# Kernel optimization log

Measured on AMD Instinct MI355X. Metric: run time of the kernel, lower is better.

Reference implementation:

```python
import jax, jax.numpy as jnp
import numpy as np

N_NODES = 200   # nlim = 50*4
EMB = 5
N_APPTYPES = 3
FEAT_IN = 50 * 52 + N_NODES  # 2800
B = 16384
E = 800


def setup_inputs() -> dict:
    key = jax.random.key(0)
    ks = jax.random.split(key, 16)
    x = jax.random.normal(ks[0], (B, 50, 52), dtype=jnp.float32)
    apps = jax.random.randint(ks[1], (B, N_NODES), 0, N_APPTYPES)
    edge_src = jax.random.randint(ks[2], (E,), 0, N_NODES)
    edge_dst = jax.random.randint(ks[3], (E,), 0, N_NODES)
    def lin(k, fan_in, fan_out):
        bound = 1.0 / np.sqrt(fan_in)
        kw, kb = jax.random.split(k)
        W = jax.random.uniform(kw, (fan_in, fan_out), minval=-bound, maxval=bound, dtype=jnp.float32)
        b = jax.random.uniform(kb, (fan_out,), minval=-bound, maxval=bound, dtype=jnp.float32)
        return W, b
    emb_table = jax.random.normal(ks[4], (N_APPTYPES, EMB), dtype=jnp.float32)
    gc_w, gc_b = lin(ks[5], EMB, 1)
    W1, b1 = lin(ks[6], FEAT_IN, 128)
    W2, b2 = lin(ks[7], 128, 128)
    W3, b3 = lin(ks[8], 128, 64)
    W4, b4 = lin(ks[9], 64, 2)
    return {"x": x, "apps": apps, "edge_src": edge_src, "edge_dst": edge_dst,
            "emb_table": emb_table, "gc_w": gc_w, "gc_b": gc_b,
            "W1": W1, "b1": b1, "W2": W2, "b2": b2,
            "W3": W3, "b3": b3, "W4": W4, "b4": b4}


def _graph_conv(h, edge_src, edge_dst, gc_w, gc_b):
    # DGL GraphConv, norm='both': D_in^{-1/2} A D_out^{-1/2} (X W) + b
    ones = jnp.ones((edge_src.shape[0],), dtype=h.dtype)
    deg_out = jnp.clip(jax.ops.segment_sum(ones, edge_src, num_segments=N_NODES), 1.0)
    deg_in = jnp.clip(jax.ops.segment_sum(ones, edge_dst, num_segments=N_NODES), 1.0)
    norm_src = deg_out ** -0.5  # [N]
    norm_dst = deg_in ** -0.5
    hw = h @ gc_w                       # [B, N, 1] (weight applied first: 5 > 1)
    msg = (hw * norm_src[None, :, None])[:, edge_src, :]      # [B, E, 1]
    agg = jnp.zeros_like(hw).at[:, edge_dst, :].add(msg)      # scatter-add over dst
    return agg * norm_dst[None, :, None] + gc_b


def reference(x, apps, edge_src, edge_dst, emb_table, gc_w, gc_b,
              W1, b1, W2, b2, W3, b3, W4, b4):
    h = emb_table[apps]                 # [B, 200, 5]; apps already length nlim -> zero-pad is no-op
    g = _graph_conv(h, edge_src, edge_dst, gc_w, gc_b)        # [B, 200, 1]
    feat = jnp.concatenate([x.reshape(x.shape[0], -1), g.reshape(g.shape[0], -1)], axis=-1)  # [B, 2800]
    a = jax.nn.softplus(feat @ W1 + b1)
    a = jax.nn.softplus(a @ W2 + b2)
    a = a @ W3 + b3
    a = a - jnp.tanh(a)                 # Tanhshrink
    out = jax.nn.sigmoid(a @ W4 + b4)   # [B, 2]
    return out
```

## Files before the change

kernel.cpp:

```cpp
#include <hip/hip_runtime.h>

#define NNODES 200
#define FEATX  2600
#define FEAT   2800
#define KPAD   2816
#define NCH    44
#define N1     128

typedef _Float16 f16;
typedef _Float16 f16x8 __attribute__((ext_vector_type(8)));
typedef float    f32x4 __attribute__((ext_vector_type(4)));

#define W1T_OFF   0u
#define W2T_OFF   720896u
#define W3T_OFF   753664u
#define WG_OFF    770048u
#define B1P_OFF   872448u
#define HW_OFF    872960u
#define WE_OFF    874816u

__device__ __forceinline__ void gl_lds16(const void* g, void* l) {
  __builtin_amdgcn_global_load_lds(
      (const __attribute__((address_space(1))) unsigned int*)g,
      (__attribute__((address_space(3))) unsigned int*)l, 16, 0, 0);
}

__global__ void p0a(const int* __restrict__ esrc, const int* __restrict__ edst,
                    const float* __restrict__ emb, const float* __restrict__ gcw,
                    const float* __restrict__ gcb, const float* __restrict__ W1,
                    const float* __restrict__ b1, char* __restrict__ ws) {
  __shared__ float dg[2][NNODES];
  const int tid = threadIdx.x;
  for (int i = tid; i < 2 * NNODES; i += 256) ((float*)dg)[i] = 0.f;
  __syncthreads();
  for (int e = tid; e < 800; e += 256) {
    atomicAdd(&dg[0][esrc[e]], 1.f);
    atomicAdd(&dg[1][edst[e]], 1.f);
  }
  __syncthreads();
  for (int i = tid; i < 2 * NNODES; i += 256) {
    float* p = (float*)dg + i;
    *p = 1.f / sqrtf(fmaxf(*p, 1.f));
  }
  if (tid < 3) {
    float s = 0.f;
    for (int q = 0; q < 5; ++q) s += emb[tid * 5 + q] * gcw[q];
    ((float*)(ws + HW_OFF))[tid] = s;
  }
  __syncthreads();
  float* we = (float*)(ws + WE_OFF);
  for (int e = tid; e < 800; e += 256)
    we[e] = dg[0][esrc[e]] * dg[1][edst[e]];
  if (tid < 128) {
    float s = 0.f;
    for (int d = 0; d < NNODES; ++d) s += W1[(FEATX + d) * N1 + tid];
    ((float*)(ws + B1P_OFF))[tid] = b1[tid] + gcb[0] * s;
  }
  float* wg = (float*)(ws + WG_OFF);
  for (int i = tid; i < NNODES * N1; i += 256) wg[i] = 0.f;
}

__global__ void p0edge(const int* __restrict__ esrc, const int* __restrict__ edst,
                       const float* __restrict__ W1, char* __restrict__ ws) {
  const float* we = (const float*)(ws + WE_OFF);
  float* wg = (float*)(ws + WG_OFF);
  const int j = threadIdx.x & 127;
  const int h = threadIdx.x >> 7;
  const int e0 = blockIdx.x * 25;
  for (int e = e0 + h; e < e0 + 25; e += 2) {
    const int s = esrc[e], d = edst[e];
    atomicAdd(&wg[s * N1 + j], we[e] * W1[(FEATX + d) * N1 + j]);
  }
}

__global__ void p0pack(const float* __restrict__ W1, const float* __restrict__ W2,
                       const float* __restrict__ W3, char* __restrict__ ws) {
  const int bid = blockIdx.x, tid = threadIdx.x;
  if (bid < NCH) {
    char* dst = ws + W1T_OFF + bid * 16384;
    const float* wg = (const float*)(ws + WG_OFF);
    const int c = tid & 127, kh = tid >> 7;
    for (int kk = kh; kk < 64; kk += 2) {
      const int k = bid * 64 + kk;
      float v;
      if (k < FEATX) v = W1[k * N1 + c];
      else if (k < FEAT) v = wg[(k - FEATX) * N1 + c];
      else v = 0.f;
      const int off = (c * 128 + kk * 2) ^ ((c & 7) << 4);
      *(f16*)(dst + off) = (f16)v;
    }
  } else if (bid == NCH) {
    char* dst = ws + W2T_OFF;
    const int c = tid & 127, kh = tid >> 7;
    for (int k = kh; k < 128; k += 2) {
      const float v = W2[k * 128 + c];
      const int off = (c * 256 + k * 2) ^ ((c & 7) << 4);
      *(f16*)(dst + off) = (f16)v;
    }
  } else {
    char* dst = ws + W3T_OFF;
    const int c = tid & 63, kh = tid >> 6;
    for (int k = kh; k < 128; k += 4) {
      const float v = W3[k * 64 + c];
      const int off = (c * 256 + k * 2) ^ ((c & 7) << 4);
      *(f16*)(dst + off) = (f16)v;
    }
  }
}

__global__ __launch_bounds__(512, 2)
void fused_main(const float* __restrict__ x, const int* __restrict__ apps,
                const char* __restrict__ ws, const float* __restrict__ b2,
                const float* __restrict__ b3, const float* __restrict__ W4,
                const float* __restrict__ b4, float* __restrict__ out) {
  __shared__ __align__(16) char lds[147456];
  char*  sA    = lds;
  char*  sB    = lds + 16384;
  char*  sW23  = lds + 49152;
  char*  sAct1 = lds + 98304;
  char*  sAct2 = lds + 114688;
  float* sAct3 = (float*)(lds + 131072);

  const int tid  = threadIdx.x;
  const int lane = tid & 63;
  const int w    = tid >> 6;
  const int lrow = lane & 15;
  const int lk   = lane >> 4;
  const int wr   = w >> 1;
  const int wc   = w & 1;
  const int blk  = blockIdx.x;

  const float* hwv = (const float*)(ws + HW_OFF);
  const float hw0 = hwv[0], hw1 = hwv[1], hw2 = hwv[2];

  const int sr = tid >> 3;
  const int sq = tid & 7;
  const float* xrow = x + (size_t)(blk * 64 + sr) * FEATX;
  const int*   arow = apps + (size_t)(blk * 64 + sr) * NNODES;

  int aoff[2], boff[2][4];
#pragma unroll
  for (int ks = 0; ks < 2; ++ks) {
    const int arow_ = wr * 16 + lrow;
    aoff[ks] = ((arow_ * 128 + ks * 64 + lk * 16) ^ ((lrow & 7) << 4));
#pragma unroll
    for (int f = 0; f < 4; ++f) {
      const int c = wc * 64 + f * 16 + lrow;
      boff[ks][f] = ((c * 128 + ks * 64 + lk * 16) ^ ((lrow & 7) << 4));
    }
  }

  const f32x4 zed = {0.f, 0.f, 0.f, 0.f};
  f32x4 acc1[4] = {zed, zed, zed, zed};

  auto loadg = [&](int k) -> uint4 {
    if (k < FEATX) return *(const uint4*)(xrow + k);
    else if (k < FEAT) return *(const uint4*)(arow + (k - FEATX));
    uint4 z; z.x = z.y = z.z = z.w = 0u; return z;
  };
  auto cvt4 = [&](int k, uint4 u, f16* h) {
    if (k < FEATX) {
      h[0] = (f16)__uint_as_float(u.x); h[1] = (f16)__uint_as_float(u.y);
      h[2] = (f16)__uint_as_float(u.z); h[3] = (f16)__uint_as_float(u.w);
    } else if (k < FEAT) {
      h[0] = (f16)(u.x == 0u ? hw0 : (u.x == 1u ? hw1 : hw2));
      h[1] = (f16)(u.y == 0u ? hw0 : (u.y == 1u ? hw1 : hw2));
      h[2] = (f16)(u.z == 0u ? hw0 : (u.z == 1u ? hw1 : hw2));
      h[3] = (f16)(u.w == 0u ? hw0 : (u.w == 1u ? hw2 == hw2 ? hw2 : hw2 : hw2));
      h[3] = (f16)(u.w == 0u ? hw0 : (u.w == 1u ? hw1 : hw2));
    } else {
      h[0] = h[1] = h[2] = h[3] = (f16)0.f;
    }
  };
  auto issueB = [&](int t, int buf) {
    const char* src = ws + W1T_OFF + (size_t)t * 16384;
    char* dst = sB + buf * 16384;
#pragma unroll
    for (int r = 0; r < 2; ++r) {
      const int o = r * 8192 + w * 1024;
      gl_lds16(src + o + lane * 16, dst + o);
    }
  };
  auto writeA = [&](int t, int buf, uint4 u0, uint4 u1) {
    const int k0 = t * 64 + sq * 8;
    union { f16x8 v; f16 h[8]; } u;
    cvt4(k0, u0, u.h);
    cvt4(k0 + 4, u1, u.h + 4);
    *(f16x8*)(sA + (buf << 13) + ((sr * 128 + sq * 16) ^ ((sr & 7) << 4))) = u.v;
  };
  auto computeC1 = [&](int buf) {
    const char* a = sA + (buf << 13);
    const char* b = sB + buf * 16384;
#pragma unroll
    for (int ks = 0; ks < 2; ++ks) {
      const f16x8 af = *(const f16x8*)(a + aoff[ks]);
#pragma unroll
      for (int f = 0; f < 4; ++f) {
        const f16x8 bf = *(const f16x8*)(b + boff[ks][f]);
        acc1[f] = __builtin_amdgcn_mfma_f32_16x16x32_f16(af, bf, acc1[f], 0, 0, 0);
      }
    }
  };

  uint4 uA0, uA1;
  uA0 = loadg(0 * 64 + sq * 8);
  uA1 = loadg(0 * 64 + sq * 8 + 4);
  issueB(0, 0);
  writeA(0, 0, uA0, uA1);
  __syncthreads();

#pragma unroll 2
  for (int t = 0; t < NCH; ++t) {
    const int buf = t & 1;
    if (t + 1 < NCH) {
      uA0 = loadg((t + 1) * 64 + sq * 8);
      uA1 = loadg((t + 1) * 64 + sq * 8 + 4);
      issueB(t + 1, buf ^ 1);
    } else {
#pragma unroll
      for (int r = 0; r < 6; ++r) {
        const int o = r * 8192 + w * 1024;
        gl_lds16(ws + W2T_OFF + o + lane * 16, sW23 + o);
      }
    }
    computeC1(buf);
    if (t + 1 < NCH) writeA(t + 1, buf ^ 1, uA0, uA1);
    __syncthreads();
  }

  const float* b1p = (const float*)(ws + B1P_OFF);
#pragma unroll
  for (int f = 0; f < 4; ++f) {
    const int col = wc * 64 + f * 16 + lrow;
    const float bb = b1p[col];
#pragma unroll
    for (int r = 0; r < 4; ++r) {
      const int row = wr * 16 + lk * 4 + r;
      float v = acc1[f][r] + bb;
      v = fmaxf(v, 0.f) + log1pf(expf(-fabsf(v)));
      *(f16*)(sAct1 + ((row * 256 + col * 2) ^ ((row & 7) << 4))) = (f16)v;
    }
  }
  __syncthreads();

  f32x4 acc2[4] = {zed, zed, zed, zed};
#pragma unroll
  for (int ks = 0; ks < 4; ++ks) {
    const int ar = wr * 16 + lrow;
    const f16x8 af = *(const f16x8*)(sAct1 + ((ar * 256 + ks * 64 + lk * 16) ^ ((lrow & 7) << 4)));
#pragma unroll
    for (int f = 0; f < 4; ++f) {
      const int c = wc * 64 + f * 16 + lrow;
      const f16x8 bf = *(const f16x8*)(sW23 + ((c * 256 + ks * 64 + lk * 16) ^ ((lrow & 7) << 4)));
      acc2[f] = __builtin_amdgcn_mfma_f32_16x16x32_f16(af, bf, acc2[f], 0, 0, 0);
    }
  }
#pragma unroll
  for (int f = 0; f < 4; ++f) {
    const int col = wc * 64 + f * 16 + lrow;
    const float bb = b2[col];
#pragma unroll
    for (int r = 0; r < 4; ++r) {
      const int row = wr * 16 + lk * 4 + r;
      float v = acc2[f][r] + bb;
      v = fmaxf(v, 0.f) + log1pf(expf(-fabsf(v)));
      *(f16*)(sAct2 + ((row * 256 + col * 2) ^ ((row & 7) << 4))) = (f16)v;
    }
  }
  __syncthreads();

  f32x4 acc3[2] = {zed, zed};
  const char* w3 = sW23 + 32768;
#pragma unroll
  for (int ks = 0; ks < 4; ++ks) {
    const int ar = wr * 16 + lrow;
    const f16x8 af = *(const f16x8*)(sAct2 + ((ar * 256 + ks * 64 + lk * 16) ^ ((lrow & 7) << 4)));
#pragma unroll
    for (int f = 0; f < 2; ++f) {
      const int c = wc * 32 + f * 16 + lrow;
      const f16x8 bf = *(const f16x8*)(w3 + ((c * 256 + ks * 64 + lk * 16) ^ ((lrow & 7) << 4)));
      acc3[f] = __builtin_amdgcn_mfma_f32_16x16x32_f16(af, bf, acc3[f], 0, 0, 0);
    }
  }
#pragma unroll
  for (int f = 0; f < 2; ++f) {
    const int col = wc * 32 + f * 16 + lrow;
    const float bb = b3[col];
#pragma unroll
    for (int r = 0; r < 4; ++r) {
      const int row = wr * 16 + lk * 4 + r;
      const float z = acc3[f][r] + bb;
      sAct3[row * 64 + col] = z - tanhf(z);
    }
  }
  __syncthreads();

  if (tid < 128) {
    const int row = tid >> 1, j = tid & 1;
    float a4 = b4[j];
#pragma unroll 8
    for (int k = 0; k < 64; ++k)
      a4 += sAct3[row * 64 + k] * W4[k * 2 + j];
    out[(size_t)(blk * 64 + row) * 2 + j] = 1.f / (1.f + expf(-a4));
  }
}

extern "C" void kernel_launch(void* const* d_in, const int* in_sizes, int n_in,
                              void* d_out, int out_size, void* d_ws, size_t ws_size,
                              hipStream_t stream) {
  const float* x    = (const float*)d_in[0];
  const int*   apps = (const int*)d_in[1];
  const int*   esrc = (const int*)d_in[2];
  const int*   edst = (const int*)d_in[3];
  const float* emb  = (const float*)d_in[4];
  const float* gcw  = (const float*)d_in[5];
  const float* gcb  = (const float*)d_in[6];
  const float* W1   = (const float*)d_in[7];
  const float* b1   = (const float*)d_in[8];
  const float* W2   = (const float*)d_in[9];
  const float* b2   = (const float*)d_in[10];
  const float* W3   = (const float*)d_in[11];
  const float* b3   = (const float*)d_in[12];
  const float* W4   = (const float*)d_in[13];
  const float* b4   = (const float*)d_in[14];
  char* ws = (char*)d_ws;
  float* out = (float*)d_out;

  hipLaunchKernelGGL(p0a, dim3(1), dim3(256), 0, stream,
                     esrc, edst, emb, gcw, gcb, W1, b1, ws);
  hipLaunchKernelGGL(p0edge, dim3(32), dim3(256), 0, stream, esrc, edst, W1, ws);
  hipLaunchKernelGGL(p0pack, dim3(46), dim3(256), 0, stream, W1, W2, W3, ws);
  hipLaunchKernelGGL(fused_main, dim3(256), dim3(512), 0, stream,
                     x, apps, ws, b2, b3, W4, b4, out);
}
```

Before: 346.3 us.

## Load A fragments directly into registers with triple-buffered B pipeline

```diff
diff --git a/kernel.cpp b/kernel.cpp
--- a/kernel.cpp
+++ b/kernel.cpp
@@ -3,7 +3,6 @@
 #define NNODES 200
 #define FEATX  2600
 #define FEAT   2800
-#define KPAD   2816
 #define NCH    44
 #define N1     128
 
@@ -25,10 +24,10 @@
       (__attribute__((address_space(3))) unsigned int*)l, 16, 0, 0);
 }
 
-__global__ void p0a(const int* __restrict__ esrc, const int* __restrict__ edst,
-                    const float* __restrict__ emb, const float* __restrict__ gcw,
-                    const float* __restrict__ gcb, const float* __restrict__ W1,
-                    const float* __restrict__ b1, char* __restrict__ ws) {
+__global__ void prep1(const int* __restrict__ esrc, const int* __restrict__ edst,
+                      const float* __restrict__ emb, const float* __restrict__ gcw,
+                      const float* __restrict__ gcb, const float* __restrict__ W1,
+                      const float* __restrict__ b1, char* __restrict__ ws) {
   __shared__ float dg[2][NNODES];
   const int tid = threadIdx.x;
   for (int i = tid; i < 2 * NNODES; i += 256) ((float*)dg)[i] = 0.f;
@@ -56,28 +55,32 @@
     for (int d = 0; d < NNODES; ++d) s += W1[(FEATX + d) * N1 + tid];
     ((float*)(ws + B1P_OFF))[tid] = b1[tid] + gcb[0] * s;
   }
-  float* wg = (float*)(ws + WG_OFF);
-  for (int i = tid; i < NNODES * N1; i += 256) wg[i] = 0.f;
-}
-
-__global__ void p0edge(const int* __restrict__ esrc, const int* __restrict__ edst,
+}
+
+__global__ void prepWg(const int* __restrict__ esrc, const int* __restrict__ edst,
                        const float* __restrict__ W1, char* __restrict__ ws) {
+  __shared__ int   se[800];
+  __shared__ short sd[800];
+  __shared__ float swe[800];
+  const int n = blockIdx.x;
+  const int j = threadIdx.x;
   const float* we = (const float*)(ws + WE_OFF);
-  float* wg = (float*)(ws + WG_OFF);
-  const int j = threadIdx.x & 127;
-  const int h = threadIdx.x >> 7;
-  const int e0 = blockIdx.x * 25;
-  for (int e = e0 + h; e < e0 + 25; e += 2) {
-    const int s = esrc[e], d = edst[e];
-    atomicAdd(&wg[s * N1 + j], we[e] * W1[(FEATX + d) * N1 + j]);
-  }
-}
-
-__global__ void p0pack(const float* __restrict__ W1, const float* __restrict__ W2,
-                       const float* __restrict__ W3, char* __restrict__ ws) {
+  for (int e = j; e < 800; e += 128) {
+    se[e] = esrc[e]; sd[e] = (short)edst[e]; swe[e] = we[e];
+  }
+  __syncthreads();
+  float acc = 0.f;
+  for (int e = 0; e < 800; ++e) {
+    if (se[e] == n) acc += swe[e] * W1[(FEATX + (int)sd[e]) * N1 + j];
+  }
+  ((float*)(ws + WG_OFF))[n * N1 + j] = acc;
+}
+
+__global__ void pack(const float* __restrict__ W1, const float* __restrict__ W2,
+                     const float* __restrict__ W3, char* __restrict__ ws) {
+  __shared__ __align__(16) char tile[32768];
   const int bid = blockIdx.x, tid = threadIdx.x;
   if (bid < NCH) {
-    char* dst = ws + W1T_OFF + bid * 16384;
     const float* wg = (const float*)(ws + WG_OFF);
     const int c = tid & 127, kh = tid >> 7;
     for (int kk = kh; kk < 64; kk += 2) {
@@ -86,25 +89,32 @@
       if (k < FEATX) v = W1[k * N1 + c];
       else if (k < FEAT) v = wg[(k - FEATX) * N1 + c];
       else v = 0.f;
-      const int off = (c * 128 + kk * 2) ^ ((c & 7) << 4);
-      *(f16*)(dst + off) = (f16)v;
-    }
+      *(f16*)(tile + ((c * 128 + kk * 2) ^ ((c & 7) << 4))) = (f16)v;
+    }
+    __syncthreads();
+    char* dst = ws + W1T_OFF + bid * 16384;
+    for (int i = 0; i < 4; ++i)
+      *(uint4*)(dst + tid * 16 + i * 4096) = *(const uint4*)(tile + tid * 16 + i * 4096);
   } else if (bid == NCH) {
-    char* dst = ws + W2T_OFF;
     const int c = tid & 127, kh = tid >> 7;
     for (int k = kh; k < 128; k += 2) {
       const float v = W2[k * 128 + c];
-      const int off = (c * 256 + k * 2) ^ ((c & 7) << 4);
-      *(f16*)(dst + off) = (f16)v;
-    }
+      *(f16*)(tile + ((c * 256 + k * 2) ^ ((c & 7) << 4))) = (f16)v;
+    }
+    __syncthreads();
+    char* dst = ws + W2T_OFF;
+    for (int i = 0; i < 8; ++i)
+      *(uint4*)(dst + tid * 16 + i * 4096) = *(const uint4*)(tile + tid * 16 + i * 4096);
   } else {
-    char* dst = ws + W3T_OFF;
     const int c = tid & 63, kh = tid >> 6;
     for (int k = kh; k < 128; k += 4) {
       const float v = W3[k * 64 + c];
-      const int off = (c * 256 + k * 2) ^ ((c & 7) << 4);
-      *(f16*)(dst + off) = (f16)v;
-    }
+      *(f16*)(tile + ((c * 256 + k * 2) ^ ((c & 7) << 4))) = (f16)v;
+    }
+    __syncthreads();
+    char* dst = ws + W3T_OFF;
+    for (int i = 0; i < 4; ++i)
+      *(uint4*)(dst + tid * 16 + i * 4096) = *(const uint4*)(tile + tid * 16 + i * 4096);
   }
 }
 
@@ -113,13 +123,11 @@
                 const char* __restrict__ ws, const float* __restrict__ b2,
                 const float* __restrict__ b3, const float* __restrict__ W4,
                 const float* __restrict__ b4, float* __restrict__ out) {
-  __shared__ __align__(16) char lds[147456];
-  char*  sA    = lds;
-  char*  sB    = lds + 16384;
-  char*  sW23  = lds + 49152;
-  char*  sAct1 = lds + 98304;
-  char*  sAct2 = lds + 114688;
-  float* sAct3 = (float*)(lds + 131072);
+  __shared__ __align__(16) char lds[81920];
+  char*  sB    = lds;
+  char*  sAct1 = lds + 49152;
+  char*  sAct2 = lds + 65536;
+  float* sAct3 = (float*)(lds + 49152);
 
   const int tid  = threadIdx.x;
   const int lane = tid & 63;
@@ -133,47 +141,24 @@
   const float* hwv = (const float*)(ws + HW_OFF);
   const float hw0 = hwv[0], hw1 = hwv[1], hw2 = hwv[2];
 
-  const int sr = tid >> 3;
-  const int sq = tid & 7;
-  const float* xrow = x + (size_t)(blk * 64 + sr) * FEATX;
-  const int*   arow = apps + (size_t)(blk * 64 + sr) * NNODES;
-
-  int aoff[2], boff[2][4];
-#pragma unroll
-  for (int ks = 0; ks < 2; ++ks) {
-    const int arow_ = wr * 16 + lrow;
-    aoff[ks] = ((arow_ * 128 + ks * 64 + lk * 16) ^ ((lrow & 7) << 4));
+  const int row_g = blk * 64 + wr * 16 + lrow;
+  const float* xrow = x + (size_t)row_g * FEATX;
+  const int*   irow = apps + (size_t)row_g * NNODES;
+
+  int boff[2][4];
+#pragma unroll
+  for (int ks = 0; ks < 2; ++ks)
 #pragma unroll
     for (int f = 0; f < 4; ++f) {
       const int c = wc * 64 + f * 16 + lrow;
       boff[ks][f] = ((c * 128 + ks * 64 + lk * 16) ^ ((lrow & 7) << 4));
     }
-  }
 
   const f32x4 zed = {0.f, 0.f, 0.f, 0.f};
   f32x4 acc1[4] = {zed, zed, zed, zed};
 
-  auto loadg = [&](int k) -> uint4 {
-    if (k < FEATX) return *(const uint4*)(xrow + k);
-    else if (k < FEAT) return *(const uint4*)(arow + (k - FEATX));
-    uint4 z; z.x = z.y = z.z = z.w = 0u; return z;
-  };
-  auto cvt4 = [&](int k, uint4 u, f16* h) {
-    if (k < FEATX) {
-      h[0] = (f16)__uint_as_float(u.x); h[1] = (f16)__uint_as_float(u.y);
-      h[2] = (f16)__uint_as_float(u.z); h[3] = (f16)__uint_as_float(u.w);
-    } else if (k < FEAT) {
-      h[0] = (f16)(u.x == 0u ? hw0 : (u.x == 1u ? hw1 : hw2));
-      h[1] = (f16)(u.y == 0u ? hw0 : (u.y == 1u ? hw1 : hw2));
-      h[2] = (f16)(u.z == 0u ? hw0 : (u.z == 1u ? hw1 : hw2));
-      h[3] = (f16)(u.w == 0u ? hw0 : (u.w == 1u ? hw2 == hw2 ? hw2 : hw2 : hw2));
-      h[3] = (f16)(u.w == 0u ? hw0 : (u.w == 1u ? hw1 : hw2));
-    } else {
-      h[0] = h[1] = h[2] = h[3] = (f16)0.f;
-    }
-  };
-  auto issueB = [&](int t, int buf) {
-    const char* src = ws + W1T_OFF + (size_t)t * 16384;
+  auto issueB = [&](int tc, int buf) {
+    const char* src = ws + W1T_OFF + (size_t)tc * 16384;
     char* dst = sB + buf * 16384;
 #pragma unroll
     for (int r = 0; r < 2; ++r) {
@@ -181,51 +166,87 @@
       gl_lds16(src + o + lane * 16, dst + o);
     }
   };
-  auto writeA = [&](int t, int buf, uint4 u0, uint4 u1) {
-    const int k0 = t * 64 + sq * 8;
-    union { f16x8 v; f16 h[8]; } u;
-    cvt4(k0, u0, u.h);
-    cvt4(k0 + 4, u1, u.h + 4);
-    *(f16x8*)(sA + (buf << 13) + ((sr * 128 + sq * 16) ^ ((sr & 7) << 4))) = u.v;
+  auto issueA = [&](int tc, uint4 (&ar)[2][2]) {
+#pragma unroll
+    for (int ks = 0; ks < 2; ++ks) {
+      const int k0 = tc * 64 + ks * 32 + lk * 8;
+      const char* p;
+      if (k0 + 8 <= FEATX)  p = (const char*)(xrow + k0);
+      else if (k0 < FEAT)   p = (const char*)(irow + (k0 - FEATX));
+      else                  p = (const char*)xrow;
+      ar[ks][0] = *(const uint4*)p;
+      ar[ks][1] = *(const uint4*)(p + 16);
+    }
   };
-  auto computeC1 = [&](int buf) {
-    const char* a = sA + (buf << 13);
+  auto cvtA = [&](int t, const uint4 (&ar)[2][2], f16x8 (&af)[2]) {
+#pragma unroll
+    for (int ks = 0; ks < 2; ++ks) {
+      const int k0 = t * 64 + ks * 32 + lk * 8;
+      union { uint4 u[2]; unsigned ui[8]; float f[8]; } d;
+      d.u[0] = ar[ks][0]; d.u[1] = ar[ks][1];
+      union { f16x8 v; f16 h[8]; } r;
+      if (k0 + 8 <= FEATX) {
+#pragma unroll
+        for (int j2 = 0; j2 < 8; ++j2) r.h[j2] = (f16)d.f[j2];
+      } else if (k0 < FEAT) {
+#pragma unroll
+        for (int j2 = 0; j2 < 8; ++j2) {
+          const unsigned a = d.ui[j2];
+          r.h[j2] = (f16)(a == 0u ? hw0 : (a == 1u ? hw1 : hw2));
+        }
+      } else {
+#pragma unroll
+        for (int j2 = 0; j2 < 8; ++j2) r.h[j2] = (f16)0.f;
+      }
+      af[ks] = r.v;
+    }
+  };
+  auto compute = [&](const f16x8 (&af)[2], int buf) {
     const char* b = sB + buf * 16384;
 #pragma unroll
-    for (int ks = 0; ks < 2; ++ks) {
-      const f16x8 af = *(const f16x8*)(a + aoff[ks]);
+    for (int ks = 0; ks < 2; ++ks)
 #pragma unroll
       for (int f = 0; f < 4; ++f) {
         const f16x8 bf = *(const f16x8*)(b + boff[ks][f]);
-        acc1[f] = __builtin_amdgcn_mfma_f32_16x16x32_f16(af, bf, acc1[f], 0, 0, 0);
+        acc1[f] = __builtin_amdgcn_mfma_f32_16x16x32_f16(af[ks], bf, acc1[f], 0, 0, 0);
       }
-    }
   };
 
-  uint4 uA0, uA1;
-  uA0 = loadg(0 * 64 + sq * 8);
-  uA1 = loadg(0 * 64 + sq * 8 + 4);
-  issueB(0, 0);
-  writeA(0, 0, uA0, uA1);
-  __syncthreads();
-
-#pragma unroll 2
-  for (int t = 0; t < NCH; ++t) {
-    const int buf = t & 1;
-    if (t + 1 < NCH) {
-      uA0 = loadg((t + 1) * 64 + sq * 8);
-      uA1 = loadg((t + 1) * 64 + sq * 8 + 4);
-      issueB(t + 1, buf ^ 1);
-    } else {
-#pragma unroll
-      for (int r = 0; r < 6; ++r) {
-        const int o = r * 8192 + w * 1024;
-        gl_lds16(ws + W2T_OFF + o + lane * 16, sW23 + o);
-      }
-    }
-    computeC1(buf);
-    if (t + 1 < NCH) writeA(t + 1, buf ^ 1, uA0, uA1);
-    __syncthreads();
+  uint4 arA[2][2], arB[2][2];
+  f16x8 af[2];
+
+  issueB(0, 0); issueA(0, arA);
+  issueB(1, 1); issueA(1, arB);
+
+  for (int t = 0; t < NCH; t += 2) {
+    {
+      asm volatile("s_waitcnt vmcnt(6)" ::: "memory");
+      __builtin_amdgcn_s_barrier();
+      __builtin_amdgcn_sched_barrier(0);
+      const int tc = (t + 2 < NCH) ? t + 2 : NCH - 1;
+      issueB(tc, (t + 2) % 3);
+      cvtA(t, arA, af);
+      issueA(tc, arA);
+      compute(af, t % 3);
+    }
+    {
+      asm volatile("s_waitcnt vmcnt(6)" ::: "memory");
+      __builtin_amdgcn_s_barrier();
+      __builtin_amdgcn_sched_barrier(0);
+      const int t1 = t + 1;
+      const int tc = (t1 + 2 < NCH) ? t1 + 2 : NCH - 1;
+      issueB(tc, (t1 + 2) % 3);
+      cvtA(t1, arB, af);
+      issueA(tc, arB);
+      compute(af, t1 % 3);
+    }
+  }
+  __syncthreads();
+
+#pragma unroll
+  for (int r = 0; r < 6; ++r) {
+    const int o = r * 8192 + w * 1024;
+    gl_lds16(ws + W2T_OFF + o + lane * 16, lds + o);
   }
 
   const float* b1p = (const float*)(ws + B1P_OFF);
@@ -247,12 +268,12 @@
 #pragma unroll
   for (int ks = 0; ks < 4; ++ks) {
     const int ar = wr * 16 + lrow;
-    const f16x8 af = *(const f16x8*)(sAct1 + ((ar * 256 + ks * 64 + lk * 16) ^ ((lrow & 7) << 4)));
+    const f16x8 a2 = *(const f16x8*)(sAct1 + ((ar * 256 + ks * 64 + lk * 16) ^ ((lrow & 7) << 4)));
 #pragma unroll
     for (int f = 0; f < 4; ++f) {
       const int c = wc * 64 + f * 16 + lrow;
-      const f16x8 bf = *(const f16x8*)(sW23 + ((c * 256 + ks * 64 + lk * 16) ^ ((lrow & 7) << 4)));
-      acc2[f] = __builtin_amdgcn_mfma_f32_16x16x32_f16(af, bf, acc2[f], 0, 0, 0);
+      const f16x8 bf = *(const f16x8*)(lds + ((c * 256 + ks * 64 + lk * 16) ^ ((lrow & 7) << 4)));
+      acc2[f] = __builtin_amdgcn_mfma_f32_16x16x32_f16(a2, bf, acc2[f], 0, 0, 0);
     }
   }
 #pragma unroll
@@ -270,16 +291,16 @@
   __syncthreads();
 
   f32x4 acc3[2] = {zed, zed};
-  const char* w3 = sW23 + 32768;
+  const char* w3p = lds + 32768;
 #pragma unroll
   for (int ks = 0; ks < 4; ++ks) {
     const int ar = wr * 16 + lrow;
-    const f16x8 af = *(const f16x8*)(sAct2 + ((ar * 256 + ks * 64 + lk * 16) ^ ((lrow & 7) << 4)));
+    const f16x8 a3 = *(const f16x8*)(sAct2 + ((ar * 256 + ks * 64 + lk * 16) ^ ((lrow & 7) << 4)));
 #pragma unroll
     for (int f = 0; f < 2; ++f) {
       const int c = wc * 32 + f * 16 + lrow;
-      const f16x8 bf = *(const f16x8*)(w3 + ((c * 256 + ks * 64 + lk * 16) ^ ((lrow & 7) << 4)));
-      acc3[f] = __builtin_amdgcn_mfma_f32_16x16x32_f16(af, bf, acc3[f], 0, 0, 0);
+      const f16x8 bf = *(const f16x8*)(w3p + ((c * 256 + ks * 64 + lk * 16) ^ ((lrow & 7) << 4)));
+      acc3[f] = __builtin_amdgcn_mfma_f32_16x16x32_f16(a3, bf, acc3[f], 0, 0, 0);
     }
   }
 #pragma unroll
@@ -326,10 +347,10 @@
   char* ws = (char*)d_ws;
   float* out = (float*)d_out;
 
-  hipLaunchKernelGGL(p0a, dim3(1), dim3(256), 0, stream,
+  hipLaunchKernelGGL(prep1, dim3(1), dim3(256), 0, stream,
                      esrc, edst, emb, gcw, gcb, W1, b1, ws);
-  hipLaunchKernelGGL(p0edge, dim3(32), dim3(256), 0, stream, esrc, edst, W1, ws);
-  hipLaunchKernelGGL(p0pack, dim3(46), dim3(256), 0, stream, W1, W2, W3, ws);
+  hipLaunchKernelGGL(prepWg, dim3(200), dim3(128), 0, stream, esrc, edst, W1, ws);
+  hipLaunchKernelGGL(pack, dim3(46), dim3(256), 0, stream, W1, W2, W3, ws);
   hipLaunchKernelGGL(fused_main, dim3(256), dim3(512), 0, stream,
                      x, apps, ws, b2, b3, W4, b4, out);
 }
```

New measurement: 391.4 us. 13.0% more time.
